# Kernel optimization log

Measured on AMD Instinct MI355X. Metric: run time of the kernel, lower is better.

The kernel has to match this reference:

```python
import jax, jax.numpy as jnp
import numpy as np

N, H, W, C_SH = 512, 256, 256, 16
FX = FY = 300.0


def setup_inputs() -> dict:
    key = jax.random.key(0)
    ks = jax.random.split(key, 6)
    xy = jax.random.uniform(ks[0], (N, 2), minval=-0.8, maxval=0.8)
    z = jax.random.uniform(ks[1], (N, 1), minval=2.0, maxval=6.0)
    xyz = jnp.concatenate([xy * z, z], axis=-1).astype(jnp.float32)  # in frustum
    opacity = jax.random.uniform(ks[2], (N, 1), minval=0.1, maxval=1.0)
    features = jax.random.normal(ks[3], (N, C_SH, 3), dtype=jnp.float32) * 0.3
    A = jax.random.normal(ks[4], (N, 3, 3), dtype=jnp.float32) * 0.05
    covariance = jnp.einsum('nij,nkj->nik', A, A) + 1e-6 * jnp.eye(3, dtype=jnp.float32)
    K = jnp.array([[FX, 0.0, W / 2], [0.0, FY, H / 2], [0.0, 0.0, 1.0]], dtype=jnp.float32)
    w2c = jnp.eye(4, dtype=jnp.float32)
    bg = jnp.zeros(3, jnp.float32)
    return {"xyz": xyz, "opacity": opacity, "features": features,
            "covariance": covariance, "K": K, "w2c": w2c, "bg": bg}


def sh_to_rgb(sh, vd):
    # sh: (N,16,3), vd: (N,3) unit view dirs; degree-3 real SH basis
    C0, C1 = 0.28209479177387814, 0.4886025119029199
    x, y, z = vd[:, 0:1], vd[:, 1:2], vd[:, 2:3]
    r = sh[:, 0] * C0
    r = r + C1 * (-y * sh[:, 1] + z * sh[:, 2] - x * sh[:, 3])
    xx, yy, zz = x * x, y * y, z * z
    xy, yz, xz = x * y, y * z, x * z
    r = r + (1.0925484305920792 * xy * sh[:, 4]
             - 1.0925484305920792 * yz * sh[:, 5]
             + 0.31539156525252005 * (2.0 * zz - xx - yy) * sh[:, 6]
             - 1.0925484305920792 * xz * sh[:, 7]
             + 0.5462742152960396 * (xx - yy) * sh[:, 8])
    r = r + (-0.5900435899266435 * y * (3.0 * xx - yy) * sh[:, 9]
             + 2.890611442640554 * xy * z * sh[:, 10]
             - 0.4570457994644658 * y * (4.0 * zz - xx - yy) * sh[:, 11]
             + 0.3731763325901154 * z * (2.0 * zz - 3.0 * xx - 3.0 * yy) * sh[:, 12]
             - 0.4570457994644658 * x * (4.0 * zz - xx - yy) * sh[:, 13]
             + 1.445305721320277 * z * (xx - yy) * sh[:, 14]
             - 0.5900435899266435 * x * (xx - 3.0 * yy) * sh[:, 15])
    return jnp.clip(r + 0.5, 0.0, 1.0)


def render_gaussians(xyz, opacity, features, covariance, K, w2c, bg):
    R, t = w2c[:3, :3], w2c[:3, 3]
    xyz_cam = xyz @ R.T + t                      # (N,3)
    depth = xyz_cam[:, 2]
    xy_h = xyz_cam @ K.T
    xy = xy_h[:, :2] / jnp.clip(xy_h[:, 2:3], 1e-8)
    cam_pos = jnp.linalg.inv(w2c)[:3, 3]
    vd = xyz - cam_pos
    vd = vd / jnp.clip(jnp.linalg.norm(vd, axis=-1, keepdims=True), 1e-12)
    rgb = sh_to_rgb(features, vd)                # (N,3)

    # 2D covariance via perspective Jacobian: Sigma2d = (J W S W^T J^T)[:2,:2] + 0.3 I
    tz = jnp.clip(xyz_cam[:, 2], 1e-8)
    tx, ty = xyz_cam[:, 0], xyz_cam[:, 1]
    fx, fy = K[0, 0], K[1, 1]
    zr = jnp.zeros_like(tz)
    tz2 = tz * tz
    J = jnp.stack([fx / tz, zr, -fx * tx / tz2,
                   zr, fy / tz, -fy * ty / tz2,
                   zr, zr, zr], axis=-1).reshape(-1, 3, 3)
    T = jnp.einsum('nij,jk->nik', J, R)
    cov_cam = jnp.einsum('nij,njk,nlk->nil', T, covariance, T)
    cov2d = cov_cam[:, :2, :2] + 0.3 * jnp.eye(2, dtype=xyz.dtype)

    margin = 256.0
    visible = ((depth > 0.01) & (xy[:, 0] > -margin) & (xy[:, 0] < W + margin)
               & (xy[:, 1] > -margin) & (xy[:, 1] < H + margin))

    a, b, d = cov2d[:, 0, 0], cov2d[:, 0, 1], cov2d[:, 1, 1]
    det = a * d - b * b
    trace = a + d
    lam_max = 0.5 * (trace + jnp.sqrt(jnp.clip(trace * trace - 4.0 * det, 0.0)))
    radii_f = 3.0 * jnp.sqrt(jnp.clip(lam_max, 1e-8))
    radii = jnp.where(visible, radii_f, 0.0)
    det_c = jnp.clip(det, 1e-10)
    inv00, inv01, inv11 = d / det_c, -b / det_c, a / det_c

    # depth sort (invisible pushed to back; they contribute zero alpha)
    order = jnp.argsort(jnp.where(visible, depth, jnp.inf))
    mx, my = xy[order, 0], xy[order, 1]
    dep, op, col = depth[order], opacity[order, 0], rgb[order]
    i00, i01, i11 = inv00[order], inv01[order], inv11[order]
    rad = jnp.clip(radii_f[order], 1.0)
    vis = visible[order]

    gx = jnp.arange(W, dtype=xyz.dtype)
    gy = jnp.arange(H, dtype=xyz.dtype)
    dx = gx[None, None, :] - mx[:, None, None]   # (N,1,W) -> bcast (N,H,W)
    dy = gy[None, :, None] - my[:, None, None]
    maha = (i00[:, None, None] * dx * dx
            + 2.0 * i01[:, None, None] * dx * dy
            + i11[:, None, None] * dy * dy)
    weight = jnp.exp(-0.5 * maha)

    # per-gaussian screen box (mirrors the int()-floored crop in the torch loop)
    xlo = jnp.floor(jnp.clip(mx - rad, 0.0, W))
    xhi = jnp.floor(jnp.clip(mx + rad + 1.0, 0.0, W))
    ylo = jnp.floor(jnp.clip(my - rad, 0.0, H))
    yhi = jnp.floor(jnp.clip(my + rad + 1.0, 0.0, H))
    inbox = ((gx[None, None, :] >= xlo[:, None, None]) & (gx[None, None, :] < xhi[:, None, None])
             & (gy[None, :, None] >= ylo[:, None, None]) & (gy[None, :, None] < yhi[:, None, None]))

    alpha = jnp.clip(op[:, None, None] * weight, 0.0, 0.99)
    alpha = jnp.where(inbox & vis[:, None, None], alpha, 0.0)   # (N,H,W)

    # front-to-back alpha compositing via exclusive cumprod in log space
    log1m = jnp.log1p(-alpha)
    logT_excl = jnp.cumsum(log1m, axis=0) - log1m
    Tn = jnp.exp(logT_excl)
    wgt = Tn * alpha                                            # (N,H,W)
    T_final = jnp.exp(logT_excl[-1] + log1m[-1])                # (H,W)

    render = jnp.einsum('nhw,nc->chw', wgt, col) + bg[:, None, None] * T_final
    depth_img = jnp.sum(wgt * dep[:, None, None], axis=0)[None]
    alpha_img = (1.0 - T_final)[None]
    return render, depth_img, alpha_img, radii


def reference(xyz, opacity, features, covariance, K, w2c, bg):
    return render_gaussians(xyz, opacity, features, covariance, K, w2c, bg)
```

## Files before the change

kernel.cpp:

```cpp
#include <hip/hip_runtime.h>
#include <math.h>

#define N_G   512
#define IMG_H 256
#define IMG_W 256


__global__ __launch_bounds__(N_G) void preprocess_sort(
    const float* __restrict__ xyz, const float* __restrict__ opacity,
    const float* __restrict__ features, const float* __restrict__ cov,
    const float* __restrict__ Km, const float* __restrict__ w2c,
    float* __restrict__ radii_out, float4* __restrict__ recs)
{
    __shared__ float skey[N_G];
    const int n = threadIdx.x;

    const float R00=w2c[0], R01=w2c[1], R02=w2c[2],  t0=w2c[3];
    const float R10=w2c[4], R11=w2c[5], R12=w2c[6],  t1=w2c[7];
    const float R20=w2c[8], R21=w2c[9], R22=w2c[10], t2=w2c[11];
    const float K00=Km[0],K01=Km[1],K02=Km[2];
    const float K10=Km[3],K11=Km[4],K12=Km[5];
    const float K20=Km[6],K21=Km[7],K22=Km[8];

    const float wx = xyz[n*3+0], wy = xyz[n*3+1], wz = xyz[n*3+2];
    const float cx = R00*wx + R01*wy + R02*wz + t0;
    const float cy = R10*wx + R11*wy + R12*wz + t1;
    const float cz = R20*wx + R21*wy + R22*wz + t2;
    const float depth = cz;

    const float xh = K00*cx + K01*cy + K02*cz;
    const float yh = K10*cx + K11*cy + K12*cz;
    const float zh = K20*cx + K21*cy + K22*cz;
    const float zc = fmaxf(zh, 1e-8f);
    const float mx = xh / zc, my = yh / zc;

    const float cpx = -(R00*t0 + R10*t1 + R20*t2);
    const float cpy = -(R01*t0 + R11*t1 + R21*t2);
    const float cpz = -(R02*t0 + R12*t1 + R22*t2);
    float vx = wx - cpx, vy = wy - cpy, vz = wz - cpz;
    const float nrm = fmaxf(sqrtf(vx*vx + vy*vy + vz*vz), 1e-12f);
    vx /= nrm; vy /= nrm; vz /= nrm;

    const float xx=vx*vx, yy=vy*vy, zz=vz*vz;
    const float sxy=vx*vy, syz=vy*vz, sxz=vx*vz;
    float sb[16];
    sb[0]  = 0.28209479177387814f;
    sb[1]  = -0.4886025119029199f*vy;
    sb[2]  =  0.4886025119029199f*vz;
    sb[3]  = -0.4886025119029199f*vx;
    sb[4]  =  1.0925484305920792f*sxy;
    sb[5]  = -1.0925484305920792f*syz;
    sb[6]  =  0.31539156525252005f*(2.f*zz - xx - yy);
    sb[7]  = -1.0925484305920792f*sxz;
    sb[8]  =  0.5462742152960396f*(xx - yy);
    sb[9]  = -0.5900435899266435f*vy*(3.f*xx - yy);
    sb[10] =  2.890611442640554f*sxy*vz;
    sb[11] = -0.4570457994644658f*vy*(4.f*zz - xx - yy);
    sb[12] =  0.3731763325901154f*vz*(2.f*zz - 3.f*xx - 3.f*yy);
    sb[13] = -0.4570457994644658f*vx*(4.f*zz - xx - yy);
    sb[14] =  1.445305721320277f*vz*(xx - yy);
    sb[15] = -0.5900435899266435f*vx*(xx - 3.f*yy);

    float cr = 0.f, cg = 0.f, cb = 0.f;
    const float* sh = &features[n*48];
    #pragma unroll
    for (int k = 0; k < 16; ++k) {
        cr += sb[k]*sh[k*3+0];
        cg += sb[k]*sh[k*3+1];
        cb += sb[k]*sh[k*3+2];
    }
    cr = fminf(fmaxf(cr + 0.5f, 0.f), 1.f);
    cg = fminf(fmaxf(cg + 0.5f, 0.f), 1.f);
    cb = fminf(fmaxf(cb + 0.5f, 0.f), 1.f);

    const float fx = K00, fy = K11;
    const float tz = fmaxf(cz, 1e-8f);
    const float tz2 = tz*tz;
    const float J00 = fx/tz,  J02 = -fx*cx/tz2;
    const float J11 = fy/tz,  J12 = -fy*cy/tz2;
    const float T00 = J00*R00 + J02*R20;
    const float T01 = J00*R01 + J02*R21;
    const float T02 = J00*R02 + J02*R22;
    const float T10 = J11*R10 + J12*R20;
    const float T11 = J11*R11 + J12*R21;
    const float T12 = J11*R12 + J12*R22;
    const float* S = &cov[n*9];
    const float u0 = S[0]*T00 + S[1]*T01 + S[2]*T02;
    const float u1 = S[3]*T00 + S[4]*T01 + S[5]*T02;
    const float u2 = S[6]*T00 + S[7]*T01 + S[8]*T02;
    const float a  = T00*u0 + T01*u1 + T02*u2 + 0.3f;
    const float bb = T10*u0 + T11*u1 + T12*u2;
    const float w0 = S[0]*T10 + S[1]*T11 + S[2]*T12;
    const float w1 = S[3]*T10 + S[4]*T11 + S[5]*T12;
    const float w2 = S[6]*T10 + S[7]*T11 + S[8]*T12;
    const float d  = T10*w0 + T11*w1 + T12*w2 + 0.3f;

    const float det   = a*d - bb*bb;
    const float trace = a + d;
    const float lam   = 0.5f*(trace + sqrtf(fmaxf(trace*trace - 4.f*det, 0.f)));
    const float radii_f = 3.f*sqrtf(fmaxf(lam, 1e-8f));

    const bool visible = (depth > 0.01f) &&
                         (mx > -256.f) && (mx < (float)IMG_W + 256.f) &&
                         (my > -256.f) && (my < (float)IMG_H + 256.f);
    radii_out[n] = visible ? radii_f : 0.f;

    const float det_c = fmaxf(det, 1e-10f);
    const float i00 =  d / det_c;
    const float i01 = -bb / det_c;
    const float i11 =  a / det_c;

    const float rad = fmaxf(radii_f, 1.f);
    float xlo = floorf(fminf(fmaxf(mx - rad,      0.f), (float)IMG_W));
    float xhi = floorf(fminf(fmaxf(mx + rad + 1.f, 0.f), (float)IMG_W));
    float ylo = floorf(fminf(fmaxf(my - rad,      0.f), (float)IMG_H));
    float yhi = floorf(fminf(fmaxf(my + rad + 1.f, 0.f), (float)IMG_H));
    if (!visible) { xlo = 1e9f; xhi = -1e9f; ylo = 1e9f; yhi = -1e9f; }

    const float key = visible ? depth : INFINITY;
    skey[n] = key;
    __syncthreads();
    int rank = 0;
    for (int j = 0; j < N_G; ++j) {
        const float kj = skey[j];
        rank += (kj < key) || (kj == key && j < n);
    }

    float4* r = &recs[rank*4];
    r[0] = make_float4(xlo, xhi, ylo, yhi);
    r[1] = make_float4(mx, my, i00, i01);
    r[2] = make_float4(i11, opacity[n], depth, 0.f);
    r[3] = make_float4(cr, cg, cb, 0.f);
}

__global__ __launch_bounds__(256) void rasterize(
    const float4* __restrict__ recs, const float* __restrict__ bg,
    float* __restrict__ out)
{
    __shared__ float4 s_rec[N_G*4];
    __shared__ int   s_idx[N_G];
    __shared__ int   s_wcnt[4];

    const int tid = threadIdx.x;
    const int lane = tid & 63, w = tid >> 6;

    const float tx0 = (float)(blockIdx.x*16);
    const float tx1 = tx0 + 16.f;
    const float ty0 = (float)(blockIdx.y*16);
    const float ty1 = ty0 + 16.f;

    int running = 0;
    #pragma unroll
    for (int c = 0; c < 2; ++c) {
        const int g = c*256 + tid;
        const float4 q0 = recs[g*4];
        const bool keep = (q0.x < tx1) && (q0.y > tx0) && (q0.z < ty1) && (q0.w > ty0);
        const unsigned long long m = __ballot(keep);
        const int pre = __popcll(m & ((1ull << lane) - 1ull));
        if (lane == 0) s_wcnt[w] = __popcll(m);
        __syncthreads();
        int off = running;
        for (int i = 0; i < w; ++i) off += s_wcnt[i];
        if (keep) s_idx[off + pre] = g;
        running += s_wcnt[0] + s_wcnt[1] + s_wcnt[2] + s_wcnt[3];
        __syncthreads();
    }
    const int cnt = running;

    for (int i = tid; i < cnt*4; i += 256) {
        const int gi = s_idx[i >> 2];
        s_rec[i] = recs[gi*4 + (i & 3)];
    }
    __syncthreads();

    const float fpx = tx0 + (float)(tid & 15);
    const float fpy = ty0 + (float)(tid >> 4);

    float T = 1.f, cr = 0.f, cg = 0.f, cb = 0.f, D = 0.f;

    if (cnt > 0) {
        float4 a0 = s_rec[0], a1 = s_rec[1], a2 = s_rec[2], a3 = s_rec[3];
        for (int g = 0; g < cnt; ++g) {
            const int nx = (g + 1 < cnt) ? (g + 1) : g;
            const float4 b0 = s_rec[4*nx+0], b1 = s_rec[4*nx+1];
            const float4 b2 = s_rec[4*nx+2], b3 = s_rec[4*nx+3];
            if (fpx >= a0.x && fpx < a0.y && fpy >= a0.z && fpy < a0.w) {
                const float dx = fpx - a1.x, dy = fpy - a1.y;
                const float maha = a1.z*dx*dx + 2.f*a1.w*dx*dy + a2.x*dy*dy;
                const float alpha = fminf(a2.y*__expf(-0.5f*maha), 0.99f);
                const float wgt = T*alpha;
                cr += wgt*a3.x; cg += wgt*a3.y; cb += wgt*a3.z; D += wgt*a2.z;
                T *= (1.f - alpha);
            }
            a0 = b0; a1 = b1; a2 = b2; a3 = b3;
            if (__all(T < 1e-7f)) break;
        }
    }

    const int p = (int)fpy*IMG_W + (int)fpx;
    const float b0 = bg[0], b1 = bg[1], b2 = bg[2];
    out[p]                 = cr + b0*T;
    out[IMG_H*IMG_W   + p] = cg + b1*T;
    out[2*IMG_H*IMG_W + p] = cb + b2*T;
    out[3*IMG_H*IMG_W + p] = D;
    out[4*IMG_H*IMG_W + p] = 1.f - T;
}

extern "C" void kernel_launch(void* const* d_in, const int* in_sizes, int n_in,
                              void* d_out, int out_size, void* d_ws, size_t ws_size,
                              hipStream_t stream) {
    const float* xyz      = (const float*)d_in[0];
    const float* opacity  = (const float*)d_in[1];
    const float* features = (const float*)d_in[2];
    const float* cov      = (const float*)d_in[3];
    const float* Km       = (const float*)d_in[4];
    const float* w2c      = (const float*)d_in[5];
    const float* bg       = (const float*)d_in[6];
    float* out = (float*)d_out;
    float4* recs = (float4*)d_ws;
    float* radii_out = out + 5*IMG_H*IMG_W;

    preprocess_sort<<<1, N_G, 0, stream>>>(xyz, opacity, features, cov, Km, w2c,
                                           radii_out, recs);
    rasterize<<<dim3(IMG_W/16, IMG_H/16), 256, 0, stream>>>(recs, bg, out);
}
```

Measured before the change: 89.14 us.

## Bulk-load all records into LDS and cull tiles via shared-memory indices

Each raster block now copies the full 32 KB record array into shared memory with fully coalesced float4 loads, plus separate bounding-box arrays, instead of issuing dependent scattered gathers of culled records. Culling is done from LDS with a single barrier-merged ballot for both halves, and the compositing loop reads records indirectly through s_idx with a two-ahead index prefetch. This removes the global gather latency and one barrier pair, at the cost of loading all records per block regardless of how many survive culling, extra LDS usage (~42 KB) that may reduce occupancy, and an extra indirection in the inner loop.

```diff
diff --git a/kernel.cpp b/kernel.cpp
--- a/kernel.cpp
+++ b/kernel.cpp
@@ -138,38 +138,45 @@
     float* __restrict__ out)
 {
     __shared__ float4 s_rec[N_G*4];
-    __shared__ int   s_idx[N_G];
-    __shared__ int   s_wcnt[4];
-
-    const int tid = threadIdx.x;
+    __shared__ float  s_xlo[N_G], s_xhi[N_G], s_ylo[N_G], s_yhi[N_G];
+    __shared__ int    s_idx[N_G];
+    __shared__ int    s_cnt[8];
+
+    const int tid  = threadIdx.x;
     const int lane = tid & 63, w = tid >> 6;
 
-    const float tx0 = (float)(blockIdx.x*16);
-    const float tx1 = tx0 + 16.f;
-    const float ty0 = (float)(blockIdx.y*16);
-    const float ty1 = ty0 + 16.f;
-
-    int running = 0;
     #pragma unroll
-    for (int c = 0; c < 2; ++c) {
-        const int g = c*256 + tid;
-        const float4 q0 = recs[g*4];
-        const bool keep = (q0.x < tx1) && (q0.y > tx0) && (q0.z < ty1) && (q0.w > ty0);
-        const unsigned long long m = __ballot(keep);
-        const int pre = __popcll(m & ((1ull << lane) - 1ull));
-        if (lane == 0) s_wcnt[w] = __popcll(m);
-        __syncthreads();
-        int off = running;
-        for (int i = 0; i < w; ++i) off += s_wcnt[i];
-        if (keep) s_idx[off + pre] = g;
-        running += s_wcnt[0] + s_wcnt[1] + s_wcnt[2] + s_wcnt[3];
-        __syncthreads();
-    }
-    const int cnt = running;
-
-    for (int i = tid; i < cnt*4; i += 256) {
-        const int gi = s_idx[i >> 2];
-        s_rec[i] = recs[gi*4 + (i & 3)];
+    for (int i = 0; i < 8; ++i) {
+        const int j = tid + i*256;
+        const float4 v = recs[j];
+        s_rec[j] = v;
+        if ((j & 3) == 0) {
+            const int gi = j >> 2;
+            s_xlo[gi] = v.x; s_xhi[gi] = v.y; s_ylo[gi] = v.z; s_yhi[gi] = v.w;
+        }
+    }
+    __syncthreads();
+
+    const float tx0 = (float)(blockIdx.x*16), tx1 = tx0 + 16.f;
+    const float ty0 = (float)(blockIdx.y*16), ty1 = ty0 + 16.f;
+
+    const int g0 = tid, g1 = tid + 256;
+    const bool k0 = (s_xlo[g0] < tx1) && (s_xhi[g0] > tx0) && (s_ylo[g0] < ty1) && (s_yhi[g0] > ty0);
+    const bool k1 = (s_xlo[g1] < tx1) && (s_xhi[g1] > tx0) && (s_ylo[g1] < ty1) && (s_yhi[g1] > ty0);
+    const unsigned long long m0 = __ballot(k0);
+    const unsigned long long m1 = __ballot(k1);
+    if (lane == 0) { s_cnt[w] = __popcll(m0); s_cnt[4+w] = __popcll(m1); }
+    __syncthreads();
+    const int c0 = s_cnt[0], c1 = s_cnt[1], c2 = s_cnt[2], c3 = s_cnt[3];
+    const int c4 = s_cnt[4], c5 = s_cnt[5], c6 = s_cnt[6], c7 = s_cnt[7];
+    const int total0 = c0 + c1 + c2 + c3;
+    const int cnt    = total0 + c4 + c5 + c6 + c7;
+    {
+        const int base0 = (w>0?c0:0) + (w>1?c1:0) + (w>2?c2:0);
+        const int base1 = total0 + (w>0?c4:0) + (w>1?c5:0) + (w>2?c6:0);
+        const unsigned long long below = (1ull << lane) - 1ull;
+        if (k0) s_idx[base0 + __popcll(m0 & below)] = g0;
+        if (k1) s_idx[base1 + __popcll(m1 & below)] = g1;
     }
     __syncthreads();
 
@@ -179,11 +186,15 @@
     float T = 1.f, cr = 0.f, cg = 0.f, cb = 0.f, D = 0.f;
 
     if (cnt > 0) {
-        float4 a0 = s_rec[0], a1 = s_rec[1], a2 = s_rec[2], a3 = s_rec[3];
+        int i_nxt = (cnt > 1) ? s_idx[1] : s_idx[0];
+        int i_cur = s_idx[0];
+        float4 a0 = s_rec[4*i_cur+0], a1 = s_rec[4*i_cur+1];
+        float4 a2 = s_rec[4*i_cur+2], a3 = s_rec[4*i_cur+3];
         for (int g = 0; g < cnt; ++g) {
-            const int nx = (g + 1 < cnt) ? (g + 1) : g;
-            const float4 b0 = s_rec[4*nx+0], b1 = s_rec[4*nx+1];
-            const float4 b2 = s_rec[4*nx+2], b3 = s_rec[4*nx+3];
+            const int gn2 = (g + 2 < cnt) ? (g + 2) : (cnt - 1);
+            const int i_n2 = s_idx[gn2];
+            const float4 b0 = s_rec[4*i_nxt+0], b1 = s_rec[4*i_nxt+1];
+            const float4 b2 = s_rec[4*i_nxt+2], b3 = s_rec[4*i_nxt+3];
             if (fpx >= a0.x && fpx < a0.y && fpy >= a0.z && fpy < a0.w) {
                 const float dx = fpx - a1.x, dy = fpy - a1.y;
                 const float maha = a1.z*dx*dx + 2.f*a1.w*dx*dy + a2.x*dy*dy;
@@ -193,6 +204,7 @@
                 T *= (1.f - alpha);
             }
             a0 = b0; a1 = b1; a2 = b2; a3 = b3;
+            i_nxt = i_n2;
             if (__all(T < 1e-7f)) break;
         }
     }
```

Result: no change. 88.62 us (-0.6%).
